# Kernel tuning notes

Hardware: AMD Instinct MI355X
Metric: run time of the kernel (lower is better)

## Reference

```python
import jax, jax.numpy as jnp
import numpy as np

NEG_INF = -9e15  # matches torch's -9000000000000000.0 mask value
LEAKY_SLOPE = 0.2  # init alpha


def setup_inputs() -> dict:
    key = jax.random.key(0)
    k1, k2, k3, k4 = jax.random.split(key, 4)
    N, dim = 4096, 128
    hidden = jax.random.normal(k1, (N, dim), dtype=jnp.float32)
    adj = jax.random.randint(k2, (N, N), 0, 5)  # relation codes 0..4
    W = jax.random.normal(k3, (4, dim), dtype=jnp.float32) * (1.0 / np.sqrt(dim))
    b = jax.random.normal(k4, (4,), dtype=jnp.float32) * 0.01
    return {"hidden": hidden, "adj": adj, "W": W, "b": b}


def reference(hidden, adj, W, b):
    # e_k[i,j] = leakyrelu(sum_d h[i,d]*h[j,d]*W[k,d] + b[k])
    # equivalent to the torch repeat/view outer-product + four dim->1 Linears,
    # computed without materializing the [N,N,dim] intermediate.
    hw = hidden[None, :, :] * W[:, None, :]               # [4, N, dim]
    e = jnp.einsum('knd,md->knm', hw, hidden) + b[:, None, None]  # [4, N, N]
    e = jax.nn.leaky_relu(e, negative_slope=LEAKY_SLOPE)
    neg = jnp.asarray(NEG_INF, dtype=e.dtype)
    alpha = jnp.where(adj == 1, e[0], neg)
    alpha = jnp.where(adj == 2, e[1], alpha)
    alpha = jnp.where(adj == 3, e[2], alpha)
    alpha = jnp.where(adj == 4, e[3], alpha)
    alpha = jax.nn.softmax(alpha, axis=-1)                # [N, N]
    return alpha @ hidden                                  # [N, dim]
```

## Files before the change

### kernel.cpp

```cpp
#include <hip/hip_runtime.h>

#define NN 4096
#define DIM 128
#define TN 32
#define TM 128
#define NTILES 16

typedef __attribute__((ext_vector_type(8))) short bf16x8;
typedef __attribute__((ext_vector_type(4))) float f32x4;

#define LSTRIDE 136
#define REGION  (128 * LSTRIDE)
#define TILE_USH (2 * REGION)
#define TILE_CHUNKS 68
#define PST 136

__device__ inline unsigned short f2bf(float x) {
    union { float f; unsigned u; } v; v.f = x;
    unsigned r = v.u + 0x7FFFu + ((v.u >> 16) & 1u);
    return (unsigned short)(r >> 16);
}

__device__ inline void dma16(const void* g, void* l) {
    __builtin_amdgcn_global_load_lds(
        (const __attribute__((address_space(1))) void*)g,
        (__attribute__((address_space(3))) void*)l,
        16, 0, 0);
}

__global__ __launch_bounds__(256) void prep_pack_kernel(
    const float* __restrict__ hidden,
    unsigned short* __restrict__ Hpack)
{
    __shared__ unsigned short T[128 * LSTRIDE];
    const int tid = threadIdx.x;
    const int t0  = blockIdx.x;
    const int m0  = t0 * TM;
    unsigned short* rowdst = Hpack + (size_t)t0 * TILE_USH;
    unsigned short* coldst = rowdst + REGION;

    #pragma unroll
    for (int it = 0; it < 16; ++it) {
        int idx = tid + 256 * it;
        int row = idx >> 5;
        int c4  = (idx & 31) * 4;
        float4 v = *(const float4*)(hidden + (size_t)(m0 + row) * DIM + c4);
        ushort4 o;
        o.x = f2bf(v.x); o.y = f2bf(v.y); o.z = f2bf(v.z); o.w = f2bf(v.w);
        *(ushort4*)(rowdst + row * LSTRIDE + c4) = o;
        T[(c4 + 0) * LSTRIDE + row] = o.x;
        T[(c4 + 1) * LSTRIDE + row] = o.y;
        T[(c4 + 2) * LSTRIDE + row] = o.z;
        T[(c4 + 3) * LSTRIDE + row] = o.w;
    }
    __syncthreads();
    #pragma unroll
    for (int it = 0; it < 8; ++it) {
        int idx = tid + 256 * it;
        int d  = idx >> 4;
        int c8 = (idx & 15) * 8;
        uint4 v = *(const uint4*)(T + d * LSTRIDE + c8);
        *(uint4*)(coldst + d * LSTRIDE + c8) = v;
    }
}

__global__ __launch_bounds__(512, 2) void gat_flash_kernel(
    const float* __restrict__ hidden,
    const unsigned short* __restrict__ Hpack,
    const int*   __restrict__ adj,
    const float* __restrict__ W,
    const float* __restrict__ bvec,
    float*       __restrict__ Opart,
    float*       __restrict__ lpart)
{
    __shared__ __align__(16) unsigned short HH[2][TILE_USH];
    __shared__ __align__(16) unsigned short Plc[TN * PST];
    __shared__ float redsum[8][16];

    const int tid  = threadIdx.x;
    const int w    = tid >> 6;
    const int lane = tid & 63;
    const int g    = lane >> 4;
    const int l15  = lane & 15;
    const int blk  = blockIdx.x;
    const int nb   = blk >> 1;
    const int half = blk & 1;
    const int n0   = nb * TN;
    const int gt0  = half * NTILES;
    const int rg   = w >> 2;
    const int ms   = w & 3;
    const int lofs = lane * 16;
    const float NEG = -9.0e15f;

    const float b0 = bvec[0], b1 = bvec[1], b2 = bvec[2], b3 = bvec[3];

    {
        const char* src = (const char*)(Hpack + (size_t)gt0 * TILE_USH);
        char* dst = (char*)&HH[0][0];
        #pragma unroll
        for (int it = 0; it < 9; ++it) {
            int chunk = it * 8 + w;
            if (chunk < TILE_CHUNKS)
                dma16(src + chunk * 1024 + lofs, dst + chunk * 1024);
        }
    }
    {
        int qr = tid >> 2;
        int r  = qr & 31;
        int d0 = (tid & 3) * 32;
        const float* hrow = hidden + (size_t)(n0 + r) * DIM + d0;
        const float* wrow = W + (qr >> 5) * DIM + d0;
        unsigned short* qdst = &HH[1][qr * LSTRIDE + d0];
        #pragma unroll
        for (int c = 0; c < 8; ++c) {
            float4 hv = *(const float4*)(hrow + 4 * c);
            float4 wv = *(const float4*)(wrow + 4 * c);
            ushort4 o;
            o.x = f2bf(hv.x * wv.x); o.y = f2bf(hv.y * wv.y);
            o.z = f2bf(hv.z * wv.z); o.w = f2bf(hv.w * wv.w);
            *(ushort4*)(qdst + 4 * c) = o;
        }
    }
    __syncthreads();

    bf16x8 Af[4][4];
    #pragma unroll
    for (int k = 0; k < 4; ++k)
        #pragma unroll
        for (int ks = 0; ks < 4; ++ks)
            Af[k][ks] = *(const bf16x8*)&HH[1][(k * 32 + rg * 16 + l15) * LSTRIDE + ks * 32 + 8 * g];
    __syncthreads();

    float lrow[4] = {0.f, 0.f, 0.f, 0.f};
    f32x4 Oacc[2];
    Oacc[0] = (f32x4){0.f, 0.f, 0.f, 0.f};
    Oacc[1] = (f32x4){0.f, 0.f, 0.f, 0.f};

    const size_t arow = (size_t)(n0 + rg * 16 + 4 * g) * NN;
    int avc[8], avn[8];
    #pragma unroll
    for (int ch = 0; ch < 2; ++ch)
        #pragma unroll
        for (int t = 0; t < 4; ++t)
            avc[ch * 4 + t] = adj[arow + (size_t)t * NN + gt0 * TM + ms * 32 + ch * 16 + l15];

    for (int tile = 0; tile < NTILES; ++tile) {
        const int cur = tile & 1;
        const int nxt = cur ^ 1;

        if (tile + 1 < NTILES) {
            const char* src = (const char*)(Hpack + (size_t)(gt0 + tile + 1) * TILE_USH);
            char* dst = (char*)&HH[nxt][0];
            #pragma unroll
            for (int it = 0; it < 9; ++it) {
                int chunk = it * 8 + w;
                if (chunk < TILE_CHUNKS)
                    dma16(src + chunk * 1024 + lofs, dst + chunk * 1024);
            }
            #pragma unroll
            for (int ch = 0; ch < 2; ++ch)
                #pragma unroll
                for (int t = 0; t < 4; ++t)
                    avn[ch * 4 + t] = adj[arow + (size_t)t * NN + (gt0 + tile + 1) * TM + ms * 32 + ch * 16 + l15];
        }

        f32x4 S[4][2];
        #pragma unroll
        for (int k = 0; k < 4; ++k) {
            S[k][0] = (f32x4){0.f, 0.f, 0.f, 0.f};
            S[k][1] = (f32x4){0.f, 0.f, 0.f, 0.f};
        }
        #pragma unroll
        for (int ks = 0; ks < 4; ++ks) {
            #pragma unroll
            for (int ch = 0; ch < 2; ++ch) {
                bf16x8 B = *(const bf16x8*)&HH[cur][(ms * 32 + ch * 16 + l15) * LSTRIDE + ks * 32 + 8 * g];
                #pragma unroll
                for (int k = 0; k < 4; ++k)
                    S[k][ch] = __builtin_amdgcn_mfma_f32_16x16x32_bf16(Af[k][ks], B, S[k][ch], 0, 0, 0);
            }
        }

        #pragma unroll
        for (int ch = 0; ch < 2; ++ch) {
            #pragma unroll
            for (int t = 0; t < 4; ++t) {
                int a = avc[ch * 4 + t];
                float s = S[0][ch][t] + b0;
                s = (a == 2) ? S[1][ch][t] + b1 : s;
                s = (a == 3) ? S[2][ch][t] + b2 : s;
                s = (a == 4) ? S[3][ch][t] + b3 : s;
                float e = fmaxf(s, 0.2f * s);
                e = (a == 0) ? NEG : e;
                float p = __expf(e);
                lrow[t] += p;
                Plc[(rg * 16 + 4 * g + t) * PST + ms * 32 + ch * 16 + l15] = f2bf(p);
            }
        }

        asm volatile("s_waitcnt lgkmcnt(0)\n\ts_barrier" ::: "memory");

        #pragma unroll
        for (int c4 = 0; c4 < 4; ++c4) {
            bf16x8 Pa = *(const bf16x8*)&Plc[(rg * 16 + l15) * PST + c4 * 32 + 8 * g];
            #pragma unroll
            for (int dt = 0; dt < 2; ++dt) {
                bf16x8 Bv = *(const bf16x8*)&HH[cur][REGION + (ms * 32 + dt * 16 + l15) * LSTRIDE + c4 * 32 + 8 * g];
                Oacc[dt] = __builtin_amdgcn_mfma_f32_16x16x32_bf16(Pa, Bv, Oacc[dt], 0, 0, 0);
            }
        }

        #pragma unroll
        for (int i = 0; i < 8; ++i) avc[i] = avn[i];
        __syncthreads();
    }

    #pragma unroll
    for (int t = 0; t < 4; ++t) {
        float v = lrow[t];
        v += __shfl_xor(v, 1); v += __shfl_xor(v, 2);
        v += __shfl_xor(v, 4); v += __shfl_xor(v, 8);
        if (l15 == 0) redsum[w][4 * g + t] = v;
    }
    __syncthreads();
    if (tid < 32) {
        int rgp = tid >> 4, rr = tid & 15;
        float s = redsum[rgp * 4 + 0][rr] + redsum[rgp * 4 + 1][rr]
                + redsum[rgp * 4 + 2][rr] + redsum[rgp * 4 + 3][rr];
        lpart[blk * 32 + tid] = s;
    }
    float* Ob = Opart + (size_t)blk * TN * DIM;
    #pragma unroll
    for (int dt = 0; dt < 2; ++dt)
        #pragma unroll
        for (int t = 0; t < 4; ++t)
            Ob[(rg * 16 + 4 * g + t) * DIM + ms * 32 + dt * 16 + l15] = Oacc[dt][t];
}

__global__ __launch_bounds__(256) void combine_kernel(
    const float* __restrict__ Opart, const float* __restrict__ lpart,
    float* __restrict__ out)
{
    int idx = blockIdx.x * 256 + threadIdx.x;
    int r = idx >> 7, d = idx & 127;
    int nb = r >> 5, rr = r & 31;
    float O0 = Opart[(size_t)(nb * 2) * (TN * DIM) + rr * 128 + d];
    float O1 = Opart[(size_t)(nb * 2 + 1) * (TN * DIM) + rr * 128 + d];
    float l0 = lpart[(nb * 2) * 32 + rr];
    float l1 = lpart[(nb * 2 + 1) * 32 + rr];
    out[idx] = (O0 + O1) / (l0 + l1);
}

extern "C" void kernel_launch(void* const* d_in, const int* in_sizes, int n_in,
                              void* d_out, int out_size, void* d_ws, size_t ws_size,
                              hipStream_t stream) {
    const float* hidden = (const float*)d_in[0];
    const int*   adj    = (const int*)d_in[1];
    const float* W      = (const float*)d_in[2];
    const float* b      = (const float*)d_in[3];
    float* out = (float*)d_out;

    char* ws = (char*)d_ws;
    unsigned short* Hpack = (unsigned short*)ws;
    float* Opart = (float*)(ws + (4u << 20));
    float* lpart = (float*)(ws + (8u << 20));

    prep_pack_kernel<<<NN / TM, 256, 0, stream>>>(hidden, Hpack);
    gat_flash_kernel<<<256, 512, 0, stream>>>(hidden, Hpack, adj, W, b, Opart, lpart);
    combine_kernel<<<NN * DIM / 256, 256, 0, stream>>>(Opart, lpart, out);
}
```

Measured before the change: 138.7 us.

## Double row tile to 64 and split columns four ways for more reuse

Each block now handles 64 query rows over a quarter of the key columns instead of 32 rows over half. Each staged H tile in LDS is reused by twice as many rows, and each warp covers a 16x64 sub-tile instead of 16x32. The goal is to halve the H reloads per block and the barriers per unit of MFMA work. The cost is more registers per warp (score, output and adjacency buffers all double), a larger LDS footprint, and a partial-output buffer twice as large, which the combine kernel now sums over four splits.

New measurement: 135.5 us. 1.02x faster.

```diff
diff --git a/kernel.cpp b/kernel.cpp
--- a/kernel.cpp
+++ b/kernel.cpp
@@ -2,9 +2,10 @@
 
 #define NN 4096
 #define DIM 128
-#define TN 32
+#define TN 64
 #define TM 128
-#define NTILES 16
+#define NSPLIT 4
+#define NTILES 8
 
 typedef __attribute__((ext_vector_type(8))) short bf16x8;
 typedef __attribute__((ext_vector_type(4))) float f32x4;
@@ -83,12 +84,12 @@
     const int g    = lane >> 4;
     const int l15  = lane & 15;
     const int blk  = blockIdx.x;
-    const int nb   = blk >> 1;
-    const int half = blk & 1;
-    const int n0   = nb * TN;
-    const int gt0  = half * NTILES;
-    const int rg   = w >> 2;
-    const int ms   = w & 3;
+    const int nbr  = blk >> 2;
+    const int q4   = blk & 3;
+    const int n0   = nbr * TN;
+    const int gt0  = q4 * NTILES;
+    const int rg   = w >> 1;
+    const int msw  = w & 1;
     const int lofs = lane * 16;
     const float NEG = -9.0e15f;
 
@@ -105,20 +106,24 @@
         }
     }
     {
-        int qr = tid >> 2;
-        int r  = qr & 31;
-        int d0 = (tid & 3) * 32;
-        const float* hrow = hidden + (size_t)(n0 + r) * DIM + d0;
-        const float* wrow = W + (qr >> 5) * DIM + d0;
-        unsigned short* qdst = &HH[1][qr * LSTRIDE + d0];
-        #pragma unroll
-        for (int c = 0; c < 8; ++c) {
-            float4 hv = *(const float4*)(hrow + 4 * c);
-            float4 wv = *(const float4*)(wrow + 4 * c);
-            ushort4 o;
-            o.x = f2bf(hv.x * wv.x); o.y = f2bf(hv.y * wv.y);
-            o.z = f2bf(hv.z * wv.z); o.w = f2bf(hv.w * wv.w);
-            *(ushort4*)(qdst + 4 * c) = o;
+        #pragma unroll
+        for (int it = 0; it < 4; ++it) {
+            int idx = tid + 512 * it;
+            int row = idx >> 3;
+            int c16 = (idx & 7) * 16;
+            int k = row >> 6, r = row & 63;
+            const float* hrow = hidden + (size_t)(n0 + r) * DIM + c16;
+            const float* wrow = W + k * DIM + c16;
+            unsigned short* qdst = &HH[1][row * LSTRIDE + c16];
+            #pragma unroll
+            for (int c = 0; c < 4; ++c) {
+                float4 hv = *(const float4*)(hrow + 4 * c);
+                float4 wv = *(const float4*)(wrow + 4 * c);
+                ushort4 o;
+                o.x = f2bf(hv.x * wv.x); o.y = f2bf(hv.y * wv.y);
+                o.z = f2bf(hv.z * wv.z); o.w = f2bf(hv.w * wv.w);
+                *(ushort4*)(qdst + 4 * c) = o;
+            }
         }
     }
     __syncthreads();
@@ -128,21 +133,21 @@
     for (int k = 0; k < 4; ++k)
         #pragma unroll
         for (int ks = 0; ks < 4; ++ks)
-            Af[k][ks] = *(const bf16x8*)&HH[1][(k * 32 + rg * 16 + l15) * LSTRIDE + ks * 32 + 8 * g];
+            Af[k][ks] = *(const bf16x8*)&HH[1][(k * 64 + rg * 16 + l15) * LSTRIDE + ks * 32 + 8 * g];
     __syncthreads();
 
     float lrow[4] = {0.f, 0.f, 0.f, 0.f};
-    f32x4 Oacc[2];
-    Oacc[0] = (f32x4){0.f, 0.f, 0.f, 0.f};
-    Oacc[1] = (f32x4){0.f, 0.f, 0.f, 0.f};
+    f32x4 Oacc[4];
+    #pragma unroll
+    for (int dt = 0; dt < 4; ++dt) Oacc[dt] = (f32x4){0.f, 0.f, 0.f, 0.f};
 
     const size_t arow = (size_t)(n0 + rg * 16 + 4 * g) * NN;
-    int avc[8], avn[8];
-    #pragma unroll
-    for (int ch = 0; ch < 2; ++ch)
+    int avc[16], avn[16];
+    #pragma unroll
+    for (int ch = 0; ch < 4; ++ch)
         #pragma unroll
         for (int t = 0; t < 4; ++t)
-            avc[ch * 4 + t] = adj[arow + (size_t)t * NN + gt0 * TM + ms * 32 + ch * 16 + l15];
+            avc[ch * 4 + t] = adj[arow + (size_t)t * NN + gt0 * TM + msw * 64 + ch * 16 + l15];
 
     for (int tile = 0; tile < NTILES; ++tile) {
         const int cur = tile & 1;
@@ -158,23 +163,23 @@
                     dma16(src + chunk * 1024 + lofs, dst + chunk * 1024);
             }
             #pragma unroll
-            for (int ch = 0; ch < 2; ++ch)
+            for (int ch = 0; ch < 4; ++ch)
                 #pragma unroll
                 for (int t = 0; t < 4; ++t)
-                    avn[ch * 4 + t] = adj[arow + (size_t)t * NN + (gt0 + tile + 1) * TM + ms * 32 + ch * 16 + l15];
-        }
-
-        f32x4 S[4][2];
-        #pragma unroll
-        for (int k = 0; k < 4; ++k) {
-            S[k][0] = (f32x4){0.f, 0.f, 0.f, 0.f};
-            S[k][1] = (f32x4){0.f, 0.f, 0.f, 0.f};
-        }
+                    avn[ch * 4 + t] = adj[arow + (size_t)t * NN + (gt0 + tile + 1) * TM + msw * 64 + ch * 16 + l15];
+        }
+
+        f32x4 S[4][4];
+        #pragma unroll
+        for (int k = 0; k < 4; ++k)
+            #pragma unroll
+            for (int ch = 0; ch < 4; ++ch)
+                S[k][ch] = (f32x4){0.f, 0.f, 0.f, 0.f};
         #pragma unroll
         for (int ks = 0; ks < 4; ++ks) {
             #pragma unroll
-            for (int ch = 0; ch < 2; ++ch) {
-                bf16x8 B = *(const bf16x8*)&HH[cur][(ms * 32 + ch * 16 + l15) * LSTRIDE + ks * 32 + 8 * g];
+            for (int ch = 0; ch < 4; ++ch) {
+                bf16x8 B = *(const bf16x8*)&HH[cur][(msw * 64 + ch * 16 + l15) * LSTRIDE + ks * 32 + 8 * g];
                 #pragma unroll
                 for (int k = 0; k < 4; ++k)
                     S[k][ch] = __builtin_amdgcn_mfma_f32_16x16x32_bf16(Af[k][ks], B, S[k][ch], 0, 0, 0);
@@ -182,7 +187,7 @@
         }
 
         #pragma unroll
-        for (int ch = 0; ch < 2; ++ch) {
+        for (int ch = 0; ch < 4; ++ch) {
             #pragma unroll
             for (int t = 0; t < 4; ++t) {
                 int a = avc[ch * 4 + t];
@@ -194,7 +199,7 @@
                 e = (a == 0) ? NEG : e;
                 float p = __expf(e);
                 lrow[t] += p;
-                Plc[(rg * 16 + 4 * g + t) * PST + ms * 32 + ch * 16 + l15] = f2bf(p);
+                Plc[(rg * 16 + 4 * g + t) * PST + msw * 64 + ch * 16 + l15] = f2bf(p);
             }
         }
 
@@ -204,14 +209,14 @@
         for (int c4 = 0; c4 < 4; ++c4) {
             bf16x8 Pa = *(const bf16x8*)&Plc[(rg * 16 + l15) * PST + c4 * 32 + 8 * g];
             #pragma unroll
-            for (int dt = 0; dt < 2; ++dt) {
-                bf16x8 Bv = *(const bf16x8*)&HH[cur][REGION + (ms * 32 + dt * 16 + l15) * LSTRIDE + c4 * 32 + 8 * g];
+            for (int dt = 0; dt < 4; ++dt) {
+                bf16x8 Bv = *(const bf16x8*)&HH[cur][REGION + (msw * 64 + dt * 16 + l15) * LSTRIDE + c4 * 32 + 8 * g];
                 Oacc[dt] = __builtin_amdgcn_mfma_f32_16x16x32_bf16(Pa, Bv, Oacc[dt], 0, 0, 0);
             }
         }
 
         #pragma unroll
-        for (int i = 0; i < 8; ++i) avc[i] = avn[i];
+        for (int i = 0; i < 16; ++i) avc[i] = avn[i];
         __syncthreads();
     }
 
@@ -223,18 +228,16 @@
         if (l15 == 0) redsum[w][4 * g + t] = v;
     }
     __syncthreads();
-    if (tid < 32) {
-        int rgp = tid >> 4, rr = tid & 15;
-        float s = redsum[rgp * 4 + 0][rr] + redsum[rgp * 4 + 1][rr]
-                + redsum[rgp * 4 + 2][rr] + redsum[rgp * 4 + 3][rr];
-        lpart[blk * 32 + tid] = s;
-    }
-    float* Ob = Opart + (size_t)blk * TN * DIM;
-    #pragma unroll
-    for (int dt = 0; dt < 2; ++dt)
+    if (tid < TN) {
+        int rg2 = tid >> 4, rr = tid & 15;
+        lpart[blk * TN + tid] = redsum[rg2 * 2 + 0][rr] + redsum[rg2 * 2 + 1][rr];
+    }
+    float* Ob = Opart + (size_t)blk * (TN * DIM);
+    #pragma unroll
+    for (int dt = 0; dt < 4; ++dt)
         #pragma unroll
         for (int t = 0; t < 4; ++t)
-            Ob[(rg * 16 + 4 * g + t) * DIM + ms * 32 + dt * 16 + l15] = Oacc[dt][t];
+            Ob[(rg * 16 + 4 * g + t) * DIM + msw * 64 + dt * 16 + l15] = Oacc[dt][t];
 }
 
 __global__ __launch_bounds__(256) void combine_kernel(
@@ -243,12 +246,14 @@
 {
     int idx = blockIdx.x * 256 + threadIdx.x;
     int r = idx >> 7, d = idx & 127;
-    int nb = r >> 5, rr = r & 31;
-    float O0 = Opart[(size_t)(nb * 2) * (TN * DIM) + rr * 128 + d];
-    float O1 = Opart[(size_t)(nb * 2 + 1) * (TN * DIM) + rr * 128 + d];
-    float l0 = lpart[(nb * 2) * 32 + rr];
-    float l1 = lpart[(nb * 2 + 1) * 32 + rr];
-    out[idx] = (O0 + O1) / (l0 + l1);
+    int nbr = r >> 6, rr = r & 63;
+    float O = 0.f, l = 0.f;
+    #pragma unroll
+    for (int q = 0; q < NSPLIT; ++q) {
+        O += Opart[(size_t)(nbr * NSPLIT + q) * (TN * DIM) + rr * 128 + d];
+        l += lpart[(nbr * NSPLIT + q) * TN + rr];
+    }
+    out[idx] = O / l;
 }
 
 extern "C" void kernel_launch(void* const* d_in, const int* in_sizes, int n_in,
@@ -263,7 +268,7 @@
     char* ws = (char*)d_ws;
     unsigned short* Hpack = (unsigned short*)ws;
     float* Opart = (float*)(ws + (4u << 20));
-    float* lpart = (float*)(ws + (8u << 20));
+    float* lpart = (float*)(ws + (12u << 20));
 
     prep_pack_kernel<<<NN / TM, 256, 0, stream>>>(hidden, Hpack);
     gat_flash_kernel<<<256, 512, 0, stream>>>(hidden, Hpack, adj, W, b, Opart, lpart);
```

## Split key range four ways and read transposed H directly from global

Applied to the files above, without the earlier changes.

The key dimension is now split across four blocks per row tile instead of two, doubling the grid to 512 blocks. The LDS double buffer keeps only the row-major tile, which halves shared memory per block and allows four blocks per CU via launch bounds. The transposed hidden values for the P·H matmul are written to a global d-major array and read straight from global/L2 inside the MFMA loop. This trades LDS capacity and DMA volume for more occupancy, at the cost of uncached-in-LDS global reads on the critical path and a larger combine step with more partial outputs.

Result: slower. 208.0 us (+49.9%).

```diff
diff --git a/kernel.cpp b/kernel.cpp
--- a/kernel.cpp
+++ b/kernel.cpp
@@ -4,15 +4,15 @@
 #define DIM 128
 #define TN 32
 #define TM 128
-#define NTILES 16
+#define NSPLIT 4
+#define NTILES 8
 
 typedef __attribute__((ext_vector_type(8))) short bf16x8;
 typedef __attribute__((ext_vector_type(4))) float f32x4;
 
 #define LSTRIDE 136
 #define REGION  (128 * LSTRIDE)
-#define TILE_USH (2 * REGION)
-#define TILE_CHUNKS 68
+#define TILE_CHUNKS 34
 #define PST 136
 
 __device__ inline unsigned short f2bf(float x) {
@@ -30,14 +30,14 @@
 
 __global__ __launch_bounds__(256) void prep_pack_kernel(
     const float* __restrict__ hidden,
-    unsigned short* __restrict__ Hpack)
+    unsigned short* __restrict__ Hpack,
+    unsigned short* __restrict__ hbt)
 {
     __shared__ unsigned short T[128 * LSTRIDE];
     const int tid = threadIdx.x;
     const int t0  = blockIdx.x;
     const int m0  = t0 * TM;
-    unsigned short* rowdst = Hpack + (size_t)t0 * TILE_USH;
-    unsigned short* coldst = rowdst + REGION;
+    unsigned short* rowdst = Hpack + (size_t)t0 * REGION;
 
     #pragma unroll
     for (int it = 0; it < 16; ++it) {
@@ -60,20 +60,21 @@
         int d  = idx >> 4;
         int c8 = (idx & 15) * 8;
         uint4 v = *(const uint4*)(T + d * LSTRIDE + c8);
-        *(uint4*)(coldst + d * LSTRIDE + c8) = v;
-    }
-}
-
-__global__ __launch_bounds__(512, 2) void gat_flash_kernel(
+        *(uint4*)(hbt + (size_t)d * NN + m0 + c8) = v;
+    }
+}
+
+__global__ __launch_bounds__(512, 4) void gat_flash_kernel(
     const float* __restrict__ hidden,
     const unsigned short* __restrict__ Hpack,
+    const unsigned short* __restrict__ hbt,
     const int*   __restrict__ adj,
     const float* __restrict__ W,
     const float* __restrict__ bvec,
     float*       __restrict__ Opart,
     float*       __restrict__ lpart)
 {
-    __shared__ __align__(16) unsigned short HH[2][TILE_USH];
+    __shared__ __align__(16) unsigned short HH[2][REGION];
     __shared__ __align__(16) unsigned short Plc[TN * PST];
     __shared__ float redsum[8][16];
 
@@ -83,10 +84,10 @@
     const int g    = lane >> 4;
     const int l15  = lane & 15;
     const int blk  = blockIdx.x;
-    const int nb   = blk >> 1;
-    const int half = blk & 1;
+    const int nb   = blk >> 2;
+    const int q4   = blk & 3;
     const int n0   = nb * TN;
-    const int gt0  = half * NTILES;
+    const int gt0  = q4 * NTILES;
     const int rg   = w >> 2;
     const int ms   = w & 3;
     const int lofs = lane * 16;
@@ -95,10 +96,10 @@
     const float b0 = bvec[0], b1 = bvec[1], b2 = bvec[2], b3 = bvec[3];
 
     {
-        const char* src = (const char*)(Hpack + (size_t)gt0 * TILE_USH);
+        const char* src = (const char*)(Hpack + (size_t)gt0 * REGION);
         char* dst = (char*)&HH[0][0];
         #pragma unroll
-        for (int it = 0; it < 9; ++it) {
+        for (int it = 0; it < 5; ++it) {
             int chunk = it * 8 + w;
             if (chunk < TILE_CHUNKS)
                 dma16(src + chunk * 1024 + lofs, dst + chunk * 1024);
@@ -147,12 +148,13 @@
     for (int tile = 0; tile < NTILES; ++tile) {
         const int cur = tile & 1;
         const int nxt = cur ^ 1;
+        const int mt0 = (gt0 + tile) * TM;
 
         if (tile + 1 < NTILES) {
-            const char* src = (const char*)(Hpack + (size_t)(gt0 + tile + 1) * TILE_USH);
+            const char* src = (const char*)(Hpack + (size_t)(gt0 + tile + 1) * REGION);
             char* dst = (char*)&HH[nxt][0];
             #pragma unroll
-            for (int it = 0; it < 9; ++it) {
+            for (int it = 0; it < 5; ++it) {
                 int chunk = it * 8 + w;
                 if (chunk < TILE_CHUNKS)
                     dma16(src + chunk * 1024 + lofs, dst + chunk * 1024);
@@ -205,7 +207,8 @@
             bf16x8 Pa = *(const bf16x8*)&Plc[(rg * 16 + l15) * PST + c4 * 32 + 8 * g];
             #pragma unroll
             for (int dt = 0; dt < 2; ++dt) {
-                bf16x8 Bv = *(const bf16x8*)&HH[cur][REGION + (ms * 32 + dt * 16 + l15) * LSTRIDE + c4 * 32 + 8 * g];
+                const unsigned short* hp = hbt + (size_t)(ms * 32 + dt * 16 + l15) * NN + mt0 + c4 * 32 + 8 * g;
+                bf16x8 Bv = *(const bf16x8*)hp;
                 Oacc[dt] = __builtin_amdgcn_mfma_f32_16x16x32_bf16(Pa, Bv, Oacc[dt], 0, 0, 0);
             }
         }
@@ -244,11 +247,13 @@
     int idx = blockIdx.x * 256 + threadIdx.x;
     int r = idx >> 7, d = idx & 127;
     int nb = r >> 5, rr = r & 31;
-    float O0 = Opart[(size_t)(nb * 2) * (TN * DIM) + rr * 128 + d];
-    float O1 = Opart[(size_t)(nb * 2 + 1) * (TN * DIM) + rr * 128 + d];
-    float l0 = lpart[(nb * 2) * 32 + rr];
-    float l1 = lpart[(nb * 2 + 1) * 32 + rr];
-    out[idx] = (O0 + O1) / (l0 + l1);
+    float O = 0.f, l = 0.f;
+    #pragma unroll
+    for (int q = 0; q < NSPLIT; ++q) {
+        O += Opart[(size_t)(nb * NSPLIT + q) * (TN * DIM) + rr * 128 + d];
+        l += lpart[(nb * NSPLIT + q) * 32 + rr];
+    }
+    out[idx] = O / l;
 }
 
 extern "C" void kernel_launch(void* const* d_in, const int* in_sizes, int n_in,
@@ -262,10 +267,11 @@
 
     char* ws = (char*)d_ws;
     unsigned short* Hpack = (unsigned short*)ws;
+    unsigned short* hbt   = (unsigned short*)(ws + (2u << 20));
     float* Opart = (float*)(ws + (4u << 20));
-    float* lpart = (float*)(ws + (8u << 20));
-
-    prep_pack_kernel<<<NN / TM, 256, 0, stream>>>(hidden, Hpack);
-    gat_flash_kernel<<<256, 512, 0, stream>>>(hidden, Hpack, adj, W, b, Opart, lpart);
+    float* lpart = (float*)(ws + (12u << 20));
+
+    prep_pack_kernel<<<NN / TM, 256, 0, stream>>>(hidden, Hpack, hbt);
+    gat_flash_kernel<<<512, 512, 0, stream>>>(hidden, Hpack, hbt, adj, W, b, Opart, lpart);
     combine_kernel<<<NN * DIM / 256, 256, 0, stream>>>(Opart, lpart, out);
 }
```
